# Kernel tuning notes

Measured on AMD Instinct MI355X. Metric: run time of the kernel, lower is better.

## Reference

```python
import jax, jax.numpy as jnp
import numpy as np

VOCAB, EMBED, HIDDEN, NUM_CLASSES, PAD_IDX = 50257, 128, 128, 4, 0
B, T = 256, 512


def setup_inputs() -> dict:
    key = jax.random.key(0)
    ks = jax.random.split(key, 10)
    x = jax.random.randint(ks[0], (B, T), 0, VOCAB)
    h0 = jnp.zeros((B, HIDDEN), dtype=jnp.float32)
    # embedding: uniform(-0.1, 0.1), pad row zeroed (matches init_weights)
    emb = jax.random.uniform(ks[1], (VOCAB, EMBED), jnp.float32, -0.1, 0.1)
    emb = emb.at[PAD_IDX].set(0.0)
    def xavier(k, shape):
        fan_out, fan_in = shape
        bound = float(np.sqrt(6.0 / (fan_in + fan_out)))
        return jax.random.uniform(k, shape, jnp.float32, -bound, bound)
    W_ih = xavier(ks[2], (HIDDEN, EMBED))      # rnn.weight_ih_l0
    W_hh = xavier(ks[3], (HIDDEN, HIDDEN))     # rnn.weight_hh_l0
    b_ih = jnp.zeros((HIDDEN,), jnp.float32)
    b_hh = jnp.zeros((HIDDEN,), jnp.float32)
    W1 = xavier(ks[4], (2 * HIDDEN, HIDDEN))   # output_layer1
    b1 = jnp.zeros((2 * HIDDEN,), jnp.float32)
    W2 = xavier(ks[5], (NUM_CLASSES, 2 * HIDDEN))  # output_layer2
    b2 = jnp.zeros((NUM_CLASSES,), jnp.float32)
    return {"x": x, "h0": h0, "emb": emb, "W_ih": W_ih, "W_hh": W_hh,
            "b_ih": b_ih, "b_hh": b_hh, "W1": W1, "b1": b1, "W2": W2, "b2": b2}


def reference(x, h0, emb, W_ih, W_hh, b_ih, b_hh, W1, b1, W2, b2):
    # Embedding lookup (dropout layers are identity in eval mode)
    embedded = emb[x]                                    # [B, T, E]
    # Precompute input projection for every step, then scan the recurrence.
    x_proj = jnp.einsum('bte,he->bth', embedded, W_ih) + b_ih + b_hh  # [B, T, H]
    x_proj_t = jnp.swapaxes(x_proj, 0, 1)                # [T, B, H]

    def step(h, xp):
        h_new = jnp.tanh(xp + h @ W_hh.T)                # [B, H]
        return h_new, None

    last_hidden, _ = jax.lax.scan(step, h0, x_proj_t)    # [B, H]
    # MLP head: Linear -> ReLU -> Linear
    hidden_mlp = jax.nn.relu(last_hidden @ W1.T + b1)    # [B, 2H]
    logits = hidden_mlp @ W2.T + b2                      # [B, C]
    return (logits, last_hidden)
```

## Files before the change

### kernel.cpp

```cpp
#include <hip/hip_runtime.h>
#include <hip/hip_bf16.h>
#include <math.h>

#define BB 256
#define TT 512
#define EE 128
#define HH 128
#define NC 4
#define MM (BB * TT)

typedef __bf16 bf16x8 __attribute__((ext_vector_type(8)));
typedef __bf16 bf16x4 __attribute__((ext_vector_type(4)));
typedef float  f32x4  __attribute__((ext_vector_type(4)));
typedef float  f32x2  __attribute__((ext_vector_type(2)));

__device__ __forceinline__ float fast_tanh(float x) {
    float t = __builtin_amdgcn_exp2f(x * 2.885390081777927f);
    return 1.f - 2.f * __builtin_amdgcn_rcpf(1.f + t);
}

template <typename XPT>
__global__ __launch_bounds__(256, 2) void embed_gemm(
    const int* __restrict__ x, const float* __restrict__ emb,
    const float* __restrict__ Wih, const float* __restrict__ bih,
    const float* __restrict__ bhh, XPT* __restrict__ xpout)
{
    const int tid = threadIdx.x;
    const int m0  = blockIdx.x * 128;

    const int LDA = 136;
    __shared__ __bf16 Ah[128 * 136];
    __shared__ __bf16 Al[128 * 136];
    __shared__ __bf16 Wh[128 * 136];
    __shared__ __bf16 Wl[128 * 136];
    __shared__ float  bias_s[128];

#pragma unroll
    for (int it = 0; it < 16; ++it) {
        int c   = it * 256 + tid;
        int row = c >> 5;
        int seg = c & 31;

        float4 wv = ((const float4*)Wih)[c];
        bf16x4 wh, wl;
        wh[0] = (__bf16)wv.x; wl[0] = (__bf16)(wv.x - (float)wh[0]);
        wh[1] = (__bf16)wv.y; wl[1] = (__bf16)(wv.y - (float)wh[1]);
        wh[2] = (__bf16)wv.z; wl[2] = (__bf16)(wv.z - (float)wh[2]);
        wh[3] = (__bf16)wv.w; wl[3] = (__bf16)(wv.w - (float)wh[3]);
        *(bf16x4*)&Wh[row * LDA + seg * 4] = wh;
        *(bf16x4*)&Wl[row * LDA + seg * 4] = wl;

        int gi = x[m0 + row];
        float4 av = ((const float4*)(emb + (size_t)gi * 128))[seg];
        bf16x4 ah, al;
        ah[0] = (__bf16)av.x; al[0] = (__bf16)(av.x - (float)ah[0]);
        ah[1] = (__bf16)av.y; al[1] = (__bf16)(av.y - (float)ah[1]);
        ah[2] = (__bf16)av.z; al[2] = (__bf16)(av.z - (float)ah[2]);
        ah[3] = (__bf16)av.w; al[3] = (__bf16)(av.w - (float)ah[3]);
        *(bf16x4*)&Ah[row * LDA + seg * 4] = ah;
        *(bf16x4*)&Al[row * LDA + seg * 4] = al;
    }
    if (tid < 128) bias_s[tid] = bih[tid] + bhh[tid];
    __syncthreads();

    const int lane = tid & 63, wid = tid >> 6;
    const int col  = lane & 15, quad = lane >> 4;

    f32x4 acc[2][8];
#pragma unroll
    for (int mt = 0; mt < 2; ++mt)
#pragma unroll
        for (int nt = 0; nt < 8; ++nt) acc[mt][nt] = f32x4{0.f, 0.f, 0.f, 0.f};

#pragma unroll
    for (int kk = 0; kk < 4; ++kk) {
        bf16x8 afh[2], afl[2];
#pragma unroll
        for (int mt = 0; mt < 2; ++mt) {
            int ro = (wid * 32 + mt * 16 + col) * LDA + kk * 32 + quad * 8;
            afh[mt] = *(const bf16x8*)&Ah[ro];
            afl[mt] = *(const bf16x8*)&Al[ro];
        }
#pragma unroll
        for (int nt = 0; nt < 8; ++nt) {
            int ro = (nt * 16 + col) * LDA + kk * 32 + quad * 8;
            bf16x8 wfh = *(const bf16x8*)&Wh[ro];
            bf16x8 wfl = *(const bf16x8*)&Wl[ro];
#pragma unroll
            for (int mt = 0; mt < 2; ++mt) {
                acc[mt][nt] = __builtin_amdgcn_mfma_f32_16x16x32_bf16(afh[mt], wfh, acc[mt][nt], 0, 0, 0);
                acc[mt][nt] = __builtin_amdgcn_mfma_f32_16x16x32_bf16(afl[mt], wfh, acc[mt][nt], 0, 0, 0);
                acc[mt][nt] = __builtin_amdgcn_mfma_f32_16x16x32_bf16(afh[mt], wfl, acc[mt][nt], 0, 0, 0);
            }
        }
    }

#pragma unroll
    for (int mt = 0; mt < 2; ++mt) {
#pragma unroll
        for (int nt = 0; nt < 8; ++nt) {
            int m = m0 + wid * 32 + mt * 16 + quad * 4;
            int n = nt * 16 + col;
            float bs = bias_s[n];
#pragma unroll
            for (int r = 0; r < 4; ++r)
                xpout[(size_t)(m + r) * 128 + n] = (XPT)(acc[mt][nt][r] + bs);
        }
    }
}

template <typename XPT>
__global__ __launch_bounds__(256, 1) void rnn_scan(
    const XPT* __restrict__ xp, const float* __restrict__ Whh,
    const float* __restrict__ h0, float* __restrict__ hlast)
{
    const int b    = blockIdx.x;
    const int tid  = threadIdx.x;
    const int q    = tid >> 6;
    const int lane = tid & 63;

    __shared__ float h_s[128];
    __shared__ float part[4 * 128];

    f32x2 w0[16], w1[16];
    {
        const float* r0 = Whh + (size_t)lane * 128 + q * 32;
        const float* r1 = Whh + (size_t)(lane + 64) * 128 + q * 32;
#pragma unroll
        for (int c = 0; c < 8; ++c) {
            float4 v0 = ((const float4*)r0)[c];
            float4 v1 = ((const float4*)r1)[c];
            w0[c * 2 + 0] = f32x2{v0.x, v0.y}; w0[c * 2 + 1] = f32x2{v0.z, v0.w};
            w1[c * 2 + 0] = f32x2{v1.x, v1.y}; w1[c * 2 + 1] = f32x2{v1.z, v1.w};
        }
    }

    if (tid < 128) h_s[tid] = h0[b * 128 + tid];

    const XPT* xpb = xp + (size_t)b * (TT * 128);
    float xv[8];
#pragma unroll
    for (int s = 0; s < 8; ++s)
        xv[s] = (tid < 128) ? (float)xpb[s * 128 + tid] : 0.f;
    __syncthreads();

    for (int tw = 0; tw < TT; tw += 8) {
#pragma unroll
        for (int ts = 0; ts < 8; ++ts) {
            f32x2 a0 = f32x2{0.f, 0.f}, a1 = f32x2{0.f, 0.f};
            const float* hq = &h_s[q * 32];
#pragma unroll
            for (int u = 0; u < 8; ++u) {
                float4 h4 = *(const float4*)&hq[u * 4];
                f32x2 hA = f32x2{h4.x, h4.y};
                f32x2 hB = f32x2{h4.z, h4.w};
                a0 += w0[u * 2 + 0] * hA;  a0 += w0[u * 2 + 1] * hB;
                a1 += w1[u * 2 + 0] * hA;  a1 += w1[u * 2 + 1] * hB;
            }
            part[q * 128 + lane]      = a0[0] + a0[1];
            part[q * 128 + 64 + lane] = a1[0] + a1[1];
            __syncthreads();
            if (tid < 128) {
                float s = (part[tid] + part[128 + tid])
                        + (part[256 + tid] + part[384 + tid]);
                h_s[tid] = fast_tanh(s + xv[ts]);
                if (tw + 8 < TT)
                    xv[ts] = (float)xpb[(size_t)(tw + 8 + ts) * 128 + tid];
            }
            __syncthreads();
        }
    }
    if (tid < 128) hlast[b * 128 + tid] = h_s[tid];
}

__global__ __launch_bounds__(256, 2) void mlp_head(
    const float* __restrict__ hlast, const float* __restrict__ W1,
    const float* __restrict__ b1, const float* __restrict__ W2,
    const float* __restrict__ b2, float* __restrict__ out)
{
    const int b = blockIdx.x, tid = threadIdx.x;
    __shared__ float h_row[128];
    __shared__ float hid[256];

    if (tid < 128) {
        float hv = hlast[b * 128 + tid];
        h_row[tid] = hv;
        out[1024 + b * 128 + tid] = hv;
    }
    __syncthreads();

    {
        float acc = b1[tid];
        const float4* wrow = (const float4*)(W1 + (size_t)tid * 128);
#pragma unroll
        for (int k4 = 0; k4 < 32; ++k4) {
            float4 wv = wrow[k4];
            acc += wv.x * h_row[k4 * 4 + 0] + wv.y * h_row[k4 * 4 + 1]
                 + wv.z * h_row[k4 * 4 + 2] + wv.w * h_row[k4 * 4 + 3];
        }
        hid[tid] = fmaxf(acc, 0.f);
    }
    __syncthreads();

    const int wv = tid >> 6, lane = tid & 63;
    float s = 0.f;
#pragma unroll
    for (int qq = 0; qq < 4; ++qq)
        s += hid[qq * 64 + lane] * W2[wv * 256 + qq * 64 + lane];
#pragma unroll
    for (int off = 32; off > 0; off >>= 1) s += __shfl_down(s, off);
    if (lane == 0) out[b * 4 + wv] = s + b2[wv];
}

extern "C" void kernel_launch(void* const* d_in, const int* in_sizes, int n_in,
                              void* d_out, int out_size, void* d_ws, size_t ws_size,
                              hipStream_t stream)
{
    const int*   x   = (const int*)d_in[0];
    const float* h0  = (const float*)d_in[1];
    const float* emb = (const float*)d_in[2];
    const float* Wih = (const float*)d_in[3];
    const float* Whh = (const float*)d_in[4];
    const float* bih = (const float*)d_in[5];
    const float* bhh = (const float*)d_in[6];
    const float* W1  = (const float*)d_in[7];
    const float* b1  = (const float*)d_in[8];
    const float* W2  = (const float*)d_in[9];
    const float* b2  = (const float*)d_in[10];
    float* out = (float*)d_out;

    const size_t xp_f32_bytes = (size_t)MM * 128 * sizeof(float);
    const size_t hl_bytes     = (size_t)BB * 128 * sizeof(float);

    if (ws_size >= xp_f32_bytes + hl_bytes) {
        float* xpw = (float*)d_ws;
        float* hl  = (float*)((char*)d_ws + xp_f32_bytes);
        embed_gemm<float><<<MM / 128, 256, 0, stream>>>(x, emb, Wih, bih, bhh, xpw);
        rnn_scan<float><<<BB, 256, 0, stream>>>(xpw, Whh, h0, hl);
        mlp_head<<<BB, 256, 0, stream>>>(hl, W1, b1, W2, b2, out);
    } else {
        __bf16* xpw = (__bf16*)d_ws;
        float*  hl  = (float*)((char*)d_ws + (size_t)MM * 128 * sizeof(__bf16));
        embed_gemm<__bf16><<<MM / 128, 256, 0, stream>>>(x, emb, Wih, bih, bhh, xpw);
        rnn_scan<__bf16><<<BB, 256, 0, stream>>>(xpw, Whh, h0, hl);
        mlp_head<<<BB, 256, 0, stream>>>(hl, W1, b1, W2, b2, out);
    }
}
```

Before: 293.8 us.

## Halve embed GEMM LDS footprint via K-split staging; vectorize RNN matvec with f32x4

The embedding GEMM now stages the K dimension in two halves of 64. This roughly halves shared memory per block, so more blocks can be resident to overlap gather latency, at the cost of an extra barrier and a second staging pass. Gather indices are cached in LDS once. The recurrent scan keeps its weights as f32x4 vectors pinned in VGPRs through an empty asm, preloads all h values before the FMAs, and uses four-wide accumulators. This is meant to cut per-step instruction count and shorten the dependency chain.

```diff
diff --git a/kernel.cpp b/kernel.cpp
--- a/kernel.cpp
+++ b/kernel.cpp
@@ -28,40 +28,18 @@
     const int tid = threadIdx.x;
     const int m0  = blockIdx.x * 128;
 
-    const int LDA = 136;
-    __shared__ __bf16 Ah[128 * 136];
-    __shared__ __bf16 Al[128 * 136];
-    __shared__ __bf16 Wh[128 * 136];
-    __shared__ __bf16 Wl[128 * 136];
+    const int LDA = 72;
+    __shared__ __bf16 Ah[128 * 72];
+    __shared__ __bf16 Al[128 * 72];
+    __shared__ __bf16 Wh[128 * 72];
+    __shared__ __bf16 Wl[128 * 72];
     __shared__ float  bias_s[128];
-
-#pragma unroll
-    for (int it = 0; it < 16; ++it) {
-        int c   = it * 256 + tid;
-        int row = c >> 5;
-        int seg = c & 31;
-
-        float4 wv = ((const float4*)Wih)[c];
-        bf16x4 wh, wl;
-        wh[0] = (__bf16)wv.x; wl[0] = (__bf16)(wv.x - (float)wh[0]);
-        wh[1] = (__bf16)wv.y; wl[1] = (__bf16)(wv.y - (float)wh[1]);
-        wh[2] = (__bf16)wv.z; wl[2] = (__bf16)(wv.z - (float)wh[2]);
-        wh[3] = (__bf16)wv.w; wl[3] = (__bf16)(wv.w - (float)wh[3]);
-        *(bf16x4*)&Wh[row * LDA + seg * 4] = wh;
-        *(bf16x4*)&Wl[row * LDA + seg * 4] = wl;
-
-        int gi = x[m0 + row];
-        float4 av = ((const float4*)(emb + (size_t)gi * 128))[seg];
-        bf16x4 ah, al;
-        ah[0] = (__bf16)av.x; al[0] = (__bf16)(av.x - (float)ah[0]);
-        ah[1] = (__bf16)av.y; al[1] = (__bf16)(av.y - (float)ah[1]);
-        ah[2] = (__bf16)av.z; al[2] = (__bf16)(av.z - (float)ah[2]);
-        ah[3] = (__bf16)av.w; al[3] = (__bf16)(av.w - (float)ah[3]);
-        *(bf16x4*)&Ah[row * LDA + seg * 4] = ah;
-        *(bf16x4*)&Al[row * LDA + seg * 4] = al;
-    }
-    if (tid < 128) bias_s[tid] = bih[tid] + bhh[tid];
-    __syncthreads();
+    __shared__ int    gix[128];
+
+    if (tid < 128) {
+        gix[tid]    = x[m0 + tid];
+        bias_s[tid] = bih[tid] + bhh[tid];
+    }
 
     const int lane = tid & 63, wid = tid >> 6;
     const int col  = lane & 15, quad = lane >> 4;
@@ -72,27 +50,60 @@
 #pragma unroll
         for (int nt = 0; nt < 8; ++nt) acc[mt][nt] = f32x4{0.f, 0.f, 0.f, 0.f};
 
-#pragma unroll
-    for (int kk = 0; kk < 4; ++kk) {
-        bf16x8 afh[2], afl[2];
-#pragma unroll
-        for (int mt = 0; mt < 2; ++mt) {
-            int ro = (wid * 32 + mt * 16 + col) * LDA + kk * 32 + quad * 8;
-            afh[mt] = *(const bf16x8*)&Ah[ro];
-            afl[mt] = *(const bf16x8*)&Al[ro];
-        }
-#pragma unroll
-        for (int nt = 0; nt < 8; ++nt) {
-            int ro = (nt * 16 + col) * LDA + kk * 32 + quad * 8;
-            bf16x8 wfh = *(const bf16x8*)&Wh[ro];
-            bf16x8 wfl = *(const bf16x8*)&Wl[ro];
+    __syncthreads();
+
+#pragma unroll
+    for (int half = 0; half < 2; ++half) {
+#pragma unroll
+        for (int it = 0; it < 8; ++it) {
+            int c   = it * 256 + tid;
+            int row = c >> 4;
+            int seg = c & 15;
+
+            float4 wv = ((const float4*)Wih)[row * 32 + half * 16 + seg];
+            bf16x4 wh, wl;
+            wh[0] = (__bf16)wv.x; wl[0] = (__bf16)(wv.x - (float)wh[0]);
+            wh[1] = (__bf16)wv.y; wl[1] = (__bf16)(wv.y - (float)wh[1]);
+            wh[2] = (__bf16)wv.z; wl[2] = (__bf16)(wv.z - (float)wh[2]);
+            wh[3] = (__bf16)wv.w; wl[3] = (__bf16)(wv.w - (float)wh[3]);
+            *(bf16x4*)&Wh[row * LDA + seg * 4] = wh;
+            *(bf16x4*)&Wl[row * LDA + seg * 4] = wl;
+
+            int gi = gix[row];
+            float4 av = ((const float4*)emb)[(size_t)gi * 32 + half * 16 + seg];
+            bf16x4 ah, al;
+            ah[0] = (__bf16)av.x; al[0] = (__bf16)(av.x - (float)ah[0]);
+            ah[1] = (__bf16)av.y; al[1] = (__bf16)(av.y - (float)ah[1]);
+            ah[2] = (__bf16)av.z; al[2] = (__bf16)(av.z - (float)ah[2]);
+            ah[3] = (__bf16)av.w; al[3] = (__bf16)(av.w - (float)ah[3]);
+            *(bf16x4*)&Ah[row * LDA + seg * 4] = ah;
+            *(bf16x4*)&Al[row * LDA + seg * 4] = al;
+        }
+        __syncthreads();
+
+#pragma unroll
+        for (int kk = 0; kk < 2; ++kk) {
+            bf16x8 afh[2], afl[2];
 #pragma unroll
             for (int mt = 0; mt < 2; ++mt) {
-                acc[mt][nt] = __builtin_amdgcn_mfma_f32_16x16x32_bf16(afh[mt], wfh, acc[mt][nt], 0, 0, 0);
-                acc[mt][nt] = __builtin_amdgcn_mfma_f32_16x16x32_bf16(afl[mt], wfh, acc[mt][nt], 0, 0, 0);
-                acc[mt][nt] = __builtin_amdgcn_mfma_f32_16x16x32_bf16(afh[mt], wfl, acc[mt][nt], 0, 0, 0);
-            }
-        }
+                int ro = (wid * 32 + mt * 16 + col) * LDA + kk * 32 + quad * 8;
+                afh[mt] = *(const bf16x8*)&Ah[ro];
+                afl[mt] = *(const bf16x8*)&Al[ro];
+            }
+#pragma unroll
+            for (int nt = 0; nt < 8; ++nt) {
+                int ro = (nt * 16 + col) * LDA + kk * 32 + quad * 8;
+                bf16x8 wfh = *(const bf16x8*)&Wh[ro];
+                bf16x8 wfl = *(const bf16x8*)&Wl[ro];
+#pragma unroll
+                for (int mt = 0; mt < 2; ++mt) {
+                    acc[mt][nt] = __builtin_amdgcn_mfma_f32_16x16x32_bf16(afh[mt], wfh, acc[mt][nt], 0, 0, 0);
+                    acc[mt][nt] = __builtin_amdgcn_mfma_f32_16x16x32_bf16(afl[mt], wfh, acc[mt][nt], 0, 0, 0);
+                    acc[mt][nt] = __builtin_amdgcn_mfma_f32_16x16x32_bf16(afh[mt], wfl, acc[mt][nt], 0, 0, 0);
+                }
+            }
+        }
+        if (half == 0) __syncthreads();
     }
 
 #pragma unroll
@@ -122,18 +133,19 @@
     __shared__ float h_s[128];
     __shared__ float part[4 * 128];
 
-    f32x2 w0[16], w1[16];
+    f32x4 wA[8], wB[8];
     {
         const float* r0 = Whh + (size_t)lane * 128 + q * 32;
         const float* r1 = Whh + (size_t)(lane + 64) * 128 + q * 32;
 #pragma unroll
         for (int c = 0; c < 8; ++c) {
-            float4 v0 = ((const float4*)r0)[c];
-            float4 v1 = ((const float4*)r1)[c];
-            w0[c * 2 + 0] = f32x2{v0.x, v0.y}; w0[c * 2 + 1] = f32x2{v0.z, v0.w};
-            w1[c * 2 + 0] = f32x2{v1.x, v1.y}; w1[c * 2 + 1] = f32x2{v1.z, v1.w};
-        }
-    }
+            wA[c] = *(const f32x4*)(r0 + c * 4);
+            wB[c] = *(const f32x4*)(r1 + c * 4);
+        }
+    }
+#pragma unroll
+    for (int c = 0; c < 8; ++c)
+        asm volatile("" : "+v"(wA[c]), "+v"(wB[c]));
 
     if (tid < 128) h_s[tid] = h0[b * 128 + tid];
 
@@ -147,18 +159,20 @@
     for (int tw = 0; tw < TT; tw += 8) {
 #pragma unroll
         for (int ts = 0; ts < 8; ++ts) {
-            f32x2 a0 = f32x2{0.f, 0.f}, a1 = f32x2{0.f, 0.f};
             const float* hq = &h_s[q * 32];
+            f32x4 h4[8];
+#pragma unroll
+            for (int u = 0; u < 8; ++u) h4[u] = *(const f32x4*)&hq[u * 4];
+
+            f32x4 aA = f32x4{0.f, 0.f, 0.f, 0.f};
+            f32x4 aB = f32x4{0.f, 0.f, 0.f, 0.f};
 #pragma unroll
             for (int u = 0; u < 8; ++u) {
-                float4 h4 = *(const float4*)&hq[u * 4];
-                f32x2 hA = f32x2{h4.x, h4.y};
-                f32x2 hB = f32x2{h4.z, h4.w};
-                a0 += w0[u * 2 + 0] * hA;  a0 += w0[u * 2 + 1] * hB;
-                a1 += w1[u * 2 + 0] * hA;  a1 += w1[u * 2 + 1] * hB;
-            }
-            part[q * 128 + lane]      = a0[0] + a0[1];
-            part[q * 128 + 64 + lane] = a1[0] + a1[1];
+                aA += wA[u] * h4[u];
+                aB += wB[u] * h4[u];
+            }
+            part[q * 128 + lane]      = (aA[0] + aA[1]) + (aA[2] + aA[3]);
+            part[q * 128 + 64 + lane] = (aB[0] + aB[1]) + (aB[2] + aB[3]);
             __syncthreads();
             if (tid < 128) {
                 float s = (part[tid] + part[128 + tid])
```

Result: faster. 272.7 us (-7.2%).
